# Optimization experiments

Hardware: AMD Instinct MI355X
Metric: run time of the kernel (lower is better)

## Reference

```python
import jax, jax.numpy as jnp
import numpy as np

D_LOGIC = 256
D_MEMORY = 256
NHEAD = 4
B, S = 2, 4096


def setup_inputs() -> dict:
    key = jax.random.key(0)
    ks = jax.random.split(key, 12)
    scale = 0.02
    x_logic = jax.random.normal(ks[0], (B, S, D_LOGIC), dtype=jnp.float32)
    x_memory = jax.random.normal(ks[1], (B, S, D_MEMORY), dtype=jnp.float32)
    mask = jax.random.randint(ks[2], (1, 1, S, S), 0, 2, dtype=jnp.int32)
    # torch nn.Linear weights are [out_features, in_features]
    Wq = jax.random.normal(ks[3], (D_LOGIC, D_LOGIC), dtype=jnp.float32) * scale
    bq = jnp.zeros((D_LOGIC,), dtype=jnp.float32)
    Wk = jax.random.normal(ks[4], (D_LOGIC, D_LOGIC), dtype=jnp.float32) * scale
    bk = jnp.zeros((D_LOGIC,), dtype=jnp.float32)
    Wv = jax.random.normal(ks[5], (D_MEMORY, D_MEMORY), dtype=jnp.float32) * scale
    bv = jnp.zeros((D_MEMORY,), dtype=jnp.float32)
    Wo = jax.random.normal(ks[6], (D_MEMORY, D_MEMORY), dtype=jnp.float32) * scale
    bo = jnp.zeros((D_MEMORY,), dtype=jnp.float32)
    return {"x_logic": x_logic, "x_memory": x_memory, "mask": mask,
            "Wq": Wq, "bq": bq, "Wk": Wk, "bk": bk,
            "Wv": Wv, "bv": bv, "Wo": Wo, "bo": bo}


def reference(x_logic, x_memory, mask, Wq, bq, Wk, bk, Wv, bv, Wo, bo):
    batch, seq, _ = x_logic.shape
    hd_l = D_LOGIC // NHEAD   # head_dim_logic
    hd_m = D_MEMORY // NHEAD  # head_dim_memory
    # Q, K from logic stream
    Q = (x_logic @ Wq.T + bq).reshape(batch, seq, NHEAD, hd_l)
    K = (x_logic @ Wk.T + bk).reshape(batch, seq, NHEAD, hd_l)
    # scores: [B, H, S, S]
    scores = jnp.einsum('bqhd,bkhd->bhqk', Q, K) / jnp.sqrt(jnp.float32(hd_l))
    scores = jnp.where(mask == 0, jnp.float32(-1e9), scores)
    attn = jax.nn.softmax(scores, axis=-1)
    # V from memory stream
    V = (x_memory @ Wv.T + bv).reshape(batch, seq, NHEAD, hd_m)
    out = jnp.einsum('bhqk,bkhd->bqhd', attn, V).reshape(batch, seq, D_MEMORY)
    return out @ Wo.T + bo
```

## Files before the change

### kernel.cpp

```cpp
#include <hip/hip_runtime.h>

#define S_  4096
#define HD_ 64
#define H_  4
#define B_  2
#define DM  256
#define NS  4
#define KSPAN (S_ / NS)
#define NITER (KSPAN / 64)

typedef __bf16 bf16x8 __attribute__((ext_vector_type(8)));
typedef __bf16 bf16x4 __attribute__((ext_vector_type(4)));
typedef float  f32x4  __attribute__((ext_vector_type(4)));
typedef unsigned long long u64;

__device__ __forceinline__ bf16x8 cvt8(const float* p) {
    float4 u0 = *reinterpret_cast<const float4*>(p);
    float4 u1 = *reinterpret_cast<const float4*>(p + 4);
    bf16x8 r = { (__bf16)u0.x, (__bf16)u0.y, (__bf16)u0.z, (__bf16)u0.w,
                 (__bf16)u1.x, (__bf16)u1.y, (__bf16)u1.z, (__bf16)u1.w };
    return r;
}

__global__ __launch_bounds__(256) void pack_kernel(const int* __restrict__ mask,
                                                   u64* __restrict__ packed,
                                                   const float* __restrict__ Wq,
                                                   const float* __restrict__ Wk,
                                                   const float* __restrict__ Wv,
                                                   const float* __restrict__ Wo,
                                                   __bf16* __restrict__ wqb,
                                                   __bf16* __restrict__ wkb,
                                                   __bf16* __restrict__ wvb,
                                                   __bf16* __restrict__ wob) {
    const int bid = blockIdx.x;
    if (bid < 2048) {
        const int gw   = bid * 4 + (threadIdx.x >> 6);
        const int lane = threadIdx.x & 63;
        const int r  = lane >> 4;
        const int ll = lane & 15;
#pragma unroll
        for (int sb = 0; sb < 2; ++sb) {
            int4 v[4];
#pragma unroll
            for (int j = 0; j < 4; ++j) {
                const int u   = gw + (sb * 4 + j) * 8192;
                const int kbb = u & 63;
                const int q0  = (u >> 6) * 4;
                v[j] = *reinterpret_cast<const int4*>(
                    mask + (size_t)(q0 + r) * S_ + kbb * 64 + ll * 4);
            }
#pragma unroll
            for (int j = 0; j < 4; ++j) {
                const int u   = gw + (sb * 4 + j) * 8192;
                const int kbb = u & 63;
                const int q0  = (u >> 6) * 4;
                const u64 b0 = __ballot(v[j].x != 0);
                const u64 b1 = __ballot(v[j].y != 0);
                const u64 b2 = __ballot(v[j].z != 0);
                const u64 b3 = __ballot(v[j].w != 0);
                if (ll == 0) {
                    const u64 word = ((b0 >> (16 * r)) & 0xFFFFull)
                                   | (((b1 >> (16 * r)) & 0xFFFFull) << 16)
                                   | (((b2 >> (16 * r)) & 0xFFFFull) << 32)
                                   | (((b3 >> (16 * r)) & 0xFFFFull) << 48);
                    packed[(size_t)kbb * S_ + q0 + r] = word;
                }
            }
        }
        return;
    }
    const int t = (bid - 2048) * 256 + threadIdx.x;
#pragma unroll
    for (int j = 0; j < 4; ++j) {
        const int idx = t + j * 16384;
        const int arr = idx >> 14, k = idx & 16383;
        const float* src = arr == 0 ? Wq : arr == 1 ? Wk : arr == 2 ? Wv : Wo;
        __bf16* dst      = arr == 0 ? wqb : arr == 1 ? wkb : arr == 2 ? wvb : wob;
        float4 v = reinterpret_cast<const float4*>(src)[k];
        bf16x4 o = { (__bf16)v.x, (__bf16)v.y, (__bf16)v.z, (__bf16)v.w };
        reinterpret_cast<bf16x4*>(dst)[k] = o;
    }
}

__global__ __launch_bounds__(256) void proj_qkv_kernel(const float* __restrict__ xl,
                                                       const float* __restrict__ xm,
                                                       const __bf16* __restrict__ wqb,
                                                       const __bf16* __restrict__ wkb,
                                                       const __bf16* __restrict__ wvb,
                                                       const float* __restrict__ bq,
                                                       const float* __restrict__ bk,
                                                       const float* __restrict__ bv,
                                                       __bf16* __restrict__ Qb,
                                                       __bf16* __restrict__ Kb,
                                                       __bf16* __restrict__ Vtb) {
    const int mode = blockIdx.z;
    const int ny   = blockIdx.y;
    const float*  X    = (mode == 2) ? xm : xl;
    const __bf16* W    = (mode == 0) ? wqb : (mode == 1) ? wkb : wvb;
    const float*  bias = (mode == 0) ? bq : (mode == 1) ? bk : bv;
    const float scale  = (mode == 0) ? 0.18033688011112042f : 1.0f;

    const int wid  = threadIdx.x >> 6;
    const int lane = threadIdx.x & 63;
    const int g = lane >> 4, c = lane & 15;
    const int m0 = blockIdx.x * 64 + wid * 16;
    const float* Xp = X + (size_t)m0 * DM;

    f32x4 acc[8];
#pragma unroll
    for (int i = 0; i < 8; ++i) acc[i] = (f32x4){0.f, 0.f, 0.f, 0.f};

#pragma unroll
    for (int kf = 0; kf < 8; ++kf) {
        bf16x8 a = cvt8(Xp + c * DM + kf * 32 + g * 8);
#pragma unroll
        for (int nt = 0; nt < 8; ++nt) {
            bf16x8 b = *reinterpret_cast<const bf16x8*>(
                W + (size_t)(ny * 128 + nt * 16 + c) * DM + kf * 32 + g * 8);
            acc[nt] = __builtin_amdgcn_mfma_f32_16x16x32_bf16(a, b, acc[nt], 0, 0, 0);
        }
    }

#pragma unroll
    for (int nt = 0; nt < 8; ++nt) {
        const int n = ny * 128 + nt * 16 + c;
        const float bs = bias[n];
        const int h = n >> 6, d = n & 63;
#pragma unroll
        for (int r = 0; r < 4; ++r) {
            const int m = m0 + g * 4 + r;
            const float v = (acc[nt][r] + bs) * scale;
            const int b_ = m >> 12, s = m & (S_ - 1);
            if (mode == 0)
                Qb[((size_t)(b_ * H_ + h) * S_ + s) * HD_ + d] = (__bf16)v;
            else if (mode == 1)
                Kb[((size_t)(b_ * H_ + h) * S_ + s) * HD_ + d] = (__bf16)v;
            else
                Vtb[((size_t)(b_ * H_ + h) * HD_ + d) * S_ + s] = (__bf16)v;
        }
    }
}

__global__ __launch_bounds__(256, 4) void attn_kernel(const __bf16* __restrict__ Q,
                                                      const __bf16* __restrict__ K,
                                                      const __bf16* __restrict__ Vt,
                                                      const u64* __restrict__ packed,
                                                      __bf16* __restrict__ Opart,
                                                      float* __restrict__ Lpart) {
    __shared__ __bf16 Kt[64][72];
    __shared__ __bf16 Vl[64][72];
    __shared__ __bf16 Pl[4][32][72];

    const int bh = blockIdx.x;
    const int sp = blockIdx.y;
    const int qt = blockIdx.z;
    const int tid  = threadIdx.x;
    const int wid  = tid >> 6;
    const int lane = tid & 63;
    const int g = lane >> 4, c = lane & 15;
    const int q0w = qt * 128 + wid * 32;

    const __bf16* Qp = Q + ((size_t)bh * S_ + q0w) * HD_;
    bf16x8 qb[2][2];
#pragma unroll
    for (int qh = 0; qh < 2; ++qh) {
        qb[qh][0] = *reinterpret_cast<const bf16x8*>(Qp + (qh * 16 + c) * HD_ + g * 8);
        qb[qh][1] = *reinterpret_cast<const bf16x8*>(Qp + (qh * 16 + c) * HD_ + 32 + g * 8);
    }

    const __bf16* Kp = K  + (size_t)bh * S_ * HD_;
    const __bf16* Vp = Vt + (size_t)bh * HD_ * S_;

    const int srow = tid >> 2;
    const int sseg = (tid & 3) * 16;

    f32x4 o[2][4];
#pragma unroll
    for (int qh = 0; qh < 2; ++qh)
#pragma unroll
        for (int i = 0; i < 4; ++i) o[qh][i] = (f32x4){0.f, 0.f, 0.f, 0.f};
    float rs[2] = {0.f, 0.f};

    const int k0 = sp * KSPAN;

    bf16x8 kr0, kr1, vr0, vr1;
    {
        const __bf16* krow = Kp + (size_t)(k0 + srow) * HD_ + sseg;
        const __bf16* vrow = Vp + (size_t)srow * S_ + k0 + sseg;
        kr0 = *reinterpret_cast<const bf16x8*>(krow);
        kr1 = *reinterpret_cast<const bf16x8*>(krow + 8);
        vr0 = *reinterpret_cast<const bf16x8*>(vrow);
        vr1 = *reinterpret_cast<const bf16x8*>(vrow + 8);
        *reinterpret_cast<bf16x8*>(&Kt[srow][sseg])     = kr0;
        *reinterpret_cast<bf16x8*>(&Kt[srow][sseg + 8]) = kr1;
        *reinterpret_cast<bf16x8*>(&Vl[srow][sseg])     = vr0;
        *reinterpret_cast<bf16x8*>(&Vl[srow][sseg + 8]) = vr1;
    }
    __syncthreads();

    for (int it = 0; it < NITER; ++it) {
        const int kb = k0 + it * 64;
        const bool more = (it + 1 < NITER);
        if (more) {
            const __bf16* krow = Kp + (size_t)(kb + 64 + srow) * HD_ + sseg;
            const __bf16* vrow = Vp + (size_t)srow * S_ + kb + 64 + sseg;
            kr0 = *reinterpret_cast<const bf16x8*>(krow);
            kr1 = *reinterpret_cast<const bf16x8*>(krow + 8);
            vr0 = *reinterpret_cast<const bf16x8*>(vrow);
            vr1 = *reinterpret_cast<const bf16x8*>(vrow + 8);
        }

        const u64 mwA = packed[(size_t)(kb >> 6) * S_ + q0w + c];
        const u64 mwB = packed[(size_t)(kb >> 6) * S_ + q0w + 16 + c];

        f32x4 st[4][2];
#pragma unroll
        for (int nt = 0; nt < 4; ++nt) {
            bf16x8 ka0 = *reinterpret_cast<const bf16x8*>(&Kt[nt * 16 + c][g * 8]);
            bf16x8 ka1 = *reinterpret_cast<const bf16x8*>(&Kt[nt * 16 + c][32 + g * 8]);
#pragma unroll
            for (int qh = 0; qh < 2; ++qh) {
                f32x4 z = (f32x4){0.f, 0.f, 0.f, 0.f};
                st[nt][qh] = __builtin_amdgcn_mfma_f32_16x16x32_bf16(ka0, qb[qh][0], z, 0, 0, 0);
                st[nt][qh] = __builtin_amdgcn_mfma_f32_16x16x32_bf16(ka1, qb[qh][1], st[nt][qh], 0, 0, 0);
            }
        }

#pragma unroll
        for (int qh = 0; qh < 2; ++qh) {
            const u64 mw = qh ? mwB : mwA;
            const unsigned wlo = (unsigned)mw, whi = (unsigned)(mw >> 32);
#pragma unroll
            for (int nt = 0; nt < 4; ++nt) {
                const unsigned sh = nt * 4 + g;
                float p0 = ((wlo >> sh) & 1u)        ? exp2f(st[nt][qh][0]) : 0.f;
                float p1 = ((wlo >> (sh + 16)) & 1u) ? exp2f(st[nt][qh][1]) : 0.f;
                float p2 = ((whi >> sh) & 1u)        ? exp2f(st[nt][qh][2]) : 0.f;
                float p3 = ((whi >> (sh + 16)) & 1u) ? exp2f(st[nt][qh][3]) : 0.f;
                rs[qh] += (p0 + p1) + (p2 + p3);
                bf16x4 pw = { (__bf16)p0, (__bf16)p1, (__bf16)p2, (__bf16)p3 };
                *reinterpret_cast<bf16x4*>(&Pl[wid][qh * 16 + c][nt * 16 + g * 4]) = pw;
            }
        }

        bf16x8 pa[2][2];
#pragma unroll
        for (int qh = 0; qh < 2; ++qh) {
            pa[qh][0] = *reinterpret_cast<const bf16x8*>(&Pl[wid][qh * 16 + c][g * 8]);
            pa[qh][1] = *reinterpret_cast<const bf16x8*>(&Pl[wid][qh * 16 + c][32 + g * 8]);
        }

#pragma unroll
        for (int nt = 0; nt < 4; ++nt) {
            bf16x8 vb0 = *reinterpret_cast<const bf16x8*>(&Vl[nt * 16 + c][g * 8]);
            bf16x8 vb1 = *reinterpret_cast<const bf16x8*>(&Vl[nt * 16 + c][32 + g * 8]);
#pragma unroll
            for (int qh = 0; qh < 2; ++qh) {
                o[qh][nt] = __builtin_amdgcn_mfma_f32_16x16x32_bf16(pa[qh][0], vb0, o[qh][nt], 0, 0, 0);
                o[qh][nt] = __builtin_amdgcn_mfma_f32_16x16x32_bf16(pa[qh][1], vb1, o[qh][nt], 0, 0, 0);
            }
        }

        __syncthreads();
        if (more) {
            *reinterpret_cast<bf16x8*>(&Kt[srow][sseg])     = kr0;
            *reinterpret_cast<bf16x8*>(&Kt[srow][sseg + 8]) = kr1;
            *reinterpret_cast<bf16x8*>(&Vl[srow][sseg])     = vr0;
            *reinterpret_cast<bf16x8*>(&Vl[srow][sseg + 8]) = vr1;
            __syncthreads();
        }
    }

#pragma unroll
    for (int qh = 0; qh < 2; ++qh) {
        rs[qh] += __shfl_xor(rs[qh], 16);
        rs[qh] += __shfl_xor(rs[qh], 32);
    }
    if (lane < 16) {
        Lpart[(size_t)(bh * NS + sp) * S_ + q0w + c]      = rs[0];
        Lpart[(size_t)(bh * NS + sp) * S_ + q0w + 16 + c] = rs[1];
    }

#pragma unroll
    for (int qh = 0; qh < 2; ++qh) {
        const size_t obase = ((size_t)(bh * NS + sp) * S_ + q0w + qh * 16) * 64;
#pragma unroll
        for (int nt = 0; nt < 4; ++nt) {
#pragma unroll
            for (int r = 0; r < 4; ++r)
                Opart[obase + (size_t)(g * 4 + r) * 64 + nt * 16 + c] = (__bf16)o[qh][nt][r];
        }
    }
}

__global__ __launch_bounds__(256) void proj_o_kernel(const __bf16* __restrict__ Opart,
                                                     const float* __restrict__ Lpart,
                                                     const __bf16* __restrict__ wob,
                                                     const float* __restrict__ bo,
                                                     float* __restrict__ out) {
    const int ny   = blockIdx.y;
    const int wid  = threadIdx.x >> 6;
    const int lane = threadIdx.x & 63;
    const int g = lane >> 4, c = lane & 15;
    const int m0 = blockIdx.x * 64 + wid * 16;

    const int row = m0 + c;
    const int b_ = row >> 12, s = row & (S_ - 1);

    f32x4 acc[8];
#pragma unroll
    for (int i = 0; i < 8; ++i) acc[i] = (f32x4){0.f, 0.f, 0.f, 0.f};

#pragma unroll
    for (int kf = 0; kf < 8; ++kf) {
        const int dcol = kf * 32 + g * 8;
        const int h = dcol >> 6, dm = dcol & 63;
        const int bh = b_ * H_ + h;
        float l = 0.f;
        float sum[8] = {0.f, 0.f, 0.f, 0.f, 0.f, 0.f, 0.f, 0.f};
#pragma unroll
        for (int sp = 0; sp < NS; ++sp) {
            l += Lpart[(size_t)(bh * NS + sp) * S_ + s];
            const size_t base = ((size_t)(bh * NS + sp) * S_ + s) * 64 + dm;
            bf16x8 p = *reinterpret_cast<const bf16x8*>(Opart + base);
#pragma unroll
            for (int j = 0; j < 8; ++j) sum[j] += (float)p[j];
        }
        const float invl = 1.0f / l;
        bf16x8 a = { (__bf16)(sum[0] * invl), (__bf16)(sum[1] * invl),
                     (__bf16)(sum[2] * invl), (__bf16)(sum[3] * invl),
                     (__bf16)(sum[4] * invl), (__bf16)(sum[5] * invl),
                     (__bf16)(sum[6] * invl), (__bf16)(sum[7] * invl) };
#pragma unroll
        for (int nt = 0; nt < 8; ++nt) {
            bf16x8 b = *reinterpret_cast<const bf16x8*>(
                wob + (size_t)(ny * 128 + nt * 16 + c) * DM + kf * 32 + g * 8);
            acc[nt] = __builtin_amdgcn_mfma_f32_16x16x32_bf16(a, b, acc[nt], 0, 0, 0);
        }
    }

#pragma unroll
    for (int nt = 0; nt < 8; ++nt) {
        const int n = ny * 128 + nt * 16 + c;
        const float bs = bo[n];
#pragma unroll
        for (int r = 0; r < 4; ++r) {
            const int m = m0 + g * 4 + r;
            out[(size_t)m * DM + n] = acc[nt][r] + bs;
        }
    }
}

extern "C" void kernel_launch(void* const* d_in, const int* in_sizes, int n_in,
                              void* d_out, int out_size, void* d_ws, size_t ws_size,
                              hipStream_t stream) {
    const float* x_logic  = (const float*)d_in[0];
    const float* x_memory = (const float*)d_in[1];
    const int*   mask     = (const int*)d_in[2];
    const float* Wq = (const float*)d_in[3];
    const float* bq = (const float*)d_in[4];
    const float* Wk = (const float*)d_in[5];
    const float* bk = (const float*)d_in[6];
    const float* Wv = (const float*)d_in[7];
    const float* bv = (const float*)d_in[8];
    const float* Wo = (const float*)d_in[9];
    const float* bo = (const float*)d_in[10];
    float* out = (float*)d_out;

    char* ws = (char*)d_ws;
    size_t off = 0;
    auto alloc = [&](size_t bytes) { char* p = ws + off; off += (bytes + 255) & ~255ull; return p; };

    const size_t NX = (size_t)B_ * S_ * DM;
    u64*    packed = (u64*)alloc((size_t)S_ * (S_ / 64) * 8);
    __bf16* wqb = (__bf16*)alloc((size_t)DM * DM * 2);
    __bf16* wkb = (__bf16*)alloc((size_t)DM * DM * 2);
    __bf16* wvb = (__bf16*)alloc((size_t)DM * DM * 2);
    __bf16* wob = (__bf16*)alloc((size_t)DM * DM * 2);
    __bf16* Qb  = (__bf16*)alloc(NX * 2);
    __bf16* Kb  = (__bf16*)alloc(NX * 2);
    __bf16* Vtb = (__bf16*)alloc(NX * 2);
    __bf16* Opart = (__bf16*)alloc((size_t)B_ * H_ * NS * S_ * HD_ * 2);
    float*  Lpart = (float*)alloc((size_t)B_ * H_ * NS * S_ * 4);

    pack_kernel<<<2112, 256, 0, stream>>>(mask, packed, Wq, Wk, Wv, Wo, wqb, wkb, wvb, wob);
    proj_qkv_kernel<<<dim3(128, 2, 3), 256, 0, stream>>>(x_logic, x_memory, wqb, wkb, wvb,
                                                         bq, bk, bv, Qb, Kb, Vtb);
    attn_kernel<<<dim3(8, NS, 32), 256, 0, stream>>>(Qb, Kb, Vtb, packed, Opart, Lpart);
    proj_o_kernel<<<dim3(128, 2), 256, 0, stream>>>(Opart, Lpart, wob, bo, out);
}
```

Baseline: 134.6 us.

## Swizzle attention LDS tiles, drop padding, raise occupancy, strength-reduce pointers

Replaces the padded 72-wide LDS tiles for K, V and P with unpadded 64-wide tiles that use an XOR swizzle on the column offset, so reads stay free of bank conflicts while LDS per block shrinks. It also raises the launch-bounds minimum from 4 to 5 blocks per CU, and turns the per-iteration global address arithmetic for K, V and mask words into incrementing pointers. The higher occupancy target may force the compiler to cut registers and spill, and the swizzle adds XOR address math to every LDS access.

Result: slower. 288.3 us (+114.2%).

```diff
diff --git a/kernel.cpp b/kernel.cpp
--- a/kernel.cpp
+++ b/kernel.cpp
@@ -141,15 +141,15 @@
     }
 }
 
-__global__ __launch_bounds__(256, 4) void attn_kernel(const __bf16* __restrict__ Q,
+__global__ __launch_bounds__(256, 5) void attn_kernel(const __bf16* __restrict__ Q,
                                                       const __bf16* __restrict__ K,
                                                       const __bf16* __restrict__ Vt,
                                                       const u64* __restrict__ packed,
                                                       __bf16* __restrict__ Opart,
                                                       float* __restrict__ Lpart) {
-    __shared__ __bf16 Kt[64][72];
-    __shared__ __bf16 Vl[64][72];
-    __shared__ __bf16 Pl[4][32][72];
+    __shared__ __bf16 Kt[64 * 64];
+    __shared__ __bf16 Vl[64 * 64];
+    __shared__ __bf16 Pl[4 * 32 * 64];
 
     const int bh = blockIdx.x;
     const int sp = blockIdx.y;
@@ -159,6 +159,7 @@
     const int lane = tid & 63;
     const int g = lane >> 4, c = lane & 15;
     const int q0w = qt * 128 + wid * 32;
+    const int swz = (c & 7) << 3;
 
     const __bf16* Qp = Q + ((size_t)bh * S_ + q0w) * HD_;
     bf16x8 qb[2][2];
@@ -173,6 +174,11 @@
 
     const int srow = tid >> 2;
     const int sseg = (tid & 3) * 16;
+    const int sswz = (srow & 7) << 3;
+    __bf16* kd0 = &Kt[srow * 64 + (sseg ^ sswz)];
+    __bf16* kd1 = &Kt[srow * 64 + ((sseg + 8) ^ sswz)];
+    __bf16* vd0 = &Vl[srow * 64 + (sseg ^ sswz)];
+    __bf16* vd1 = &Vl[srow * 64 + ((sseg + 8) ^ sswz)];
 
     f32x4 o[2][4];
 #pragma unroll
@@ -191,33 +197,37 @@
         kr1 = *reinterpret_cast<const bf16x8*>(krow + 8);
         vr0 = *reinterpret_cast<const bf16x8*>(vrow);
         vr1 = *reinterpret_cast<const bf16x8*>(vrow + 8);
-        *reinterpret_cast<bf16x8*>(&Kt[srow][sseg])     = kr0;
-        *reinterpret_cast<bf16x8*>(&Kt[srow][sseg + 8]) = kr1;
-        *reinterpret_cast<bf16x8*>(&Vl[srow][sseg])     = vr0;
-        *reinterpret_cast<bf16x8*>(&Vl[srow][sseg + 8]) = vr1;
-    }
+        *reinterpret_cast<bf16x8*>(kd0) = kr0;
+        *reinterpret_cast<bf16x8*>(kd1) = kr1;
+        *reinterpret_cast<bf16x8*>(vd0) = vr0;
+        *reinterpret_cast<bf16x8*>(vd1) = vr1;
+    }
+    const __bf16* kst = Kp + (size_t)(k0 + 64 + srow) * HD_ + sseg;
+    const __bf16* vst = Vp + (size_t)srow * S_ + k0 + 64 + sseg;
+    const u64*    mp  = packed + (size_t)(k0 >> 6) * S_ + q0w;
     __syncthreads();
 
     for (int it = 0; it < NITER; ++it) {
-        const int kb = k0 + it * 64;
         const bool more = (it + 1 < NITER);
         if (more) {
-            const __bf16* krow = Kp + (size_t)(kb + 64 + srow) * HD_ + sseg;
-            const __bf16* vrow = Vp + (size_t)srow * S_ + kb + 64 + sseg;
-            kr0 = *reinterpret_cast<const bf16x8*>(krow);
-            kr1 = *reinterpret_cast<const bf16x8*>(krow + 8);
-            vr0 = *reinterpret_cast<const bf16x8*>(vrow);
-            vr1 = *reinterpret_cast<const bf16x8*>(vrow + 8);
-        }
-
-        const u64 mwA = packed[(size_t)(kb >> 6) * S_ + q0w + c];
-        const u64 mwB = packed[(size_t)(kb >> 6) * S_ + q0w + 16 + c];
+            kr0 = *reinterpret_cast<const bf16x8*>(kst);
+            kr1 = *reinterpret_cast<const bf16x8*>(kst + 8);
+            vr0 = *reinterpret_cast<const bf16x8*>(vst);
+            vr1 = *reinterpret_cast<const bf16x8*>(vst + 8);
+            kst += (size_t)64 * HD_;
+            vst += 64;
+        }
+
+        const u64 mwA = mp[c];
+        const u64 mwB = mp[16 + c];
+        mp += S_;
 
         f32x4 st[4][2];
 #pragma unroll
         for (int nt = 0; nt < 4; ++nt) {
-            bf16x8 ka0 = *reinterpret_cast<const bf16x8*>(&Kt[nt * 16 + c][g * 8]);
-            bf16x8 ka1 = *reinterpret_cast<const bf16x8*>(&Kt[nt * 16 + c][32 + g * 8]);
+            const int krow = (nt * 16 + c) * 64;
+            bf16x8 ka0 = *reinterpret_cast<const bf16x8*>(&Kt[krow + ((g * 8) ^ swz)]);
+            bf16x8 ka1 = *reinterpret_cast<const bf16x8*>(&Kt[krow + ((32 + g * 8) ^ swz)]);
 #pragma unroll
             for (int qh = 0; qh < 2; ++qh) {
                 f32x4 z = (f32x4){0.f, 0.f, 0.f, 0.f};
@@ -230,6 +240,7 @@
         for (int qh = 0; qh < 2; ++qh) {
             const u64 mw = qh ? mwB : mwA;
             const unsigned wlo = (unsigned)mw, whi = (unsigned)(mw >> 32);
+            const int prow = (wid * 32 + qh * 16 + c) * 64;
 #pragma unroll
             for (int nt = 0; nt < 4; ++nt) {
                 const unsigned sh = nt * 4 + g;
@@ -239,21 +250,23 @@
                 float p3 = ((whi >> (sh + 16)) & 1u) ? exp2f(st[nt][qh][3]) : 0.f;
                 rs[qh] += (p0 + p1) + (p2 + p3);
                 bf16x4 pw = { (__bf16)p0, (__bf16)p1, (__bf16)p2, (__bf16)p3 };
-                *reinterpret_cast<bf16x4*>(&Pl[wid][qh * 16 + c][nt * 16 + g * 4]) = pw;
+                *reinterpret_cast<bf16x4*>(&Pl[prow + ((nt * 16 + g * 4) ^ swz)]) = pw;
             }
         }
 
         bf16x8 pa[2][2];
 #pragma unroll
         for (int qh = 0; qh < 2; ++qh) {
-            pa[qh][0] = *reinterpret_cast<const bf16x8*>(&Pl[wid][qh * 16 + c][g * 8]);
-            pa[qh][1] = *reinterpret_cast<const bf16x8*>(&Pl[wid][qh * 16 + c][32 + g * 8]);
+            const int prow = (wid * 32 + qh * 16 + c) * 64;
+            pa[qh][0] = *reinterpret_cast<const bf16x8*>(&Pl[prow + ((g * 8) ^ swz)]);
+            pa[qh][1] = *reinterpret_cast<const bf16x8*>(&Pl[prow + ((32 + g * 8) ^ swz)]);
         }
 
 #pragma unroll
         for (int nt = 0; nt < 4; ++nt) {
-            bf16x8 vb0 = *reinterpret_cast<const bf16x8*>(&Vl[nt * 16 + c][g * 8]);
-            bf16x8 vb1 = *reinterpret_cast<const bf16x8*>(&Vl[nt * 16 + c][32 + g * 8]);
+            const int vrow = (nt * 16 + c) * 64;
+            bf16x8 vb0 = *reinterpret_cast<const bf16x8*>(&Vl[vrow + ((g * 8) ^ swz)]);
+            bf16x8 vb1 = *reinterpret_cast<const bf16x8*>(&Vl[vrow + ((32 + g * 8) ^ swz)]);
 #pragma unroll
             for (int qh = 0; qh < 2; ++qh) {
                 o[qh][nt] = __builtin_amdgcn_mfma_f32_16x16x32_bf16(pa[qh][0], vb0, o[qh][nt], 0, 0, 0);
@@ -263,10 +276,10 @@
 
         __syncthreads();
         if (more) {
-            *reinterpret_cast<bf16x8*>(&Kt[srow][sseg])     = kr0;
-            *reinterpret_cast<bf16x8*>(&Kt[srow][sseg + 8]) = kr1;
-            *reinterpret_cast<bf16x8*>(&Vl[srow][sseg])     = vr0;
-            *reinterpret_cast<bf16x8*>(&Vl[srow][sseg + 8]) = vr1;
+            *reinterpret_cast<bf16x8*>(kd0) = kr0;
+            *reinterpret_cast<bf16x8*>(kd1) = kr1;
+            *reinterpret_cast<bf16x8*>(vd0) = vr0;
+            *reinterpret_cast<bf16x8*>(vd1) = vr1;
             __syncthreads();
         }
     }
```
